# Performance work log

Hardware: AMD Instinct MI355X
Metric: run time of the kernel (lower is better)

The kernel has to match this reference:

```python
import jax, jax.numpy as jnp
import numpy as np

N_USER = 100000
N_ITEM = 100000
SUPP = 10000
B = 1024
L = 50
S = 256
H = 4
E = 64
HID = 64


def setup_inputs() -> dict:
    key = jax.random.key(0)
    ks = jax.random.split(key, 32)
    f32 = jnp.float32
    inp = {}
    # forward int args
    inp["x"] = jax.random.randint(ks[0], (B, 2), 0, N_USER)
    inp["src_his"] = jax.random.randint(ks[1], (B, L), 0, N_ITEM)
    inp["src_hl"] = jax.random.randint(ks[2], (B,), 0, L)
    inp["tgt_his"] = jax.random.randint(ks[3], (B, L), 0, N_ITEM)
    inp["tgt_hl"] = jax.random.randint(ks[4], (B,), 0, L)
    # precomputed neighbor sampling: [2 get_user_emb calls, H heads, B, S]
    inp["sample_idx"] = jax.random.randint(ks[5], (2, H, B, S), 0, SUPP)
    inp["supp_users"] = jax.random.randint(ks[6], (SUPP,), 0, N_USER)
    # embedding tables (xavier-ish small scale)
    inp["src_user_emb"] = jax.random.normal(ks[7], (N_USER, E), f32) * 0.1
    inp["src_item_emb"] = jax.random.normal(ks[8], (N_ITEM, E), f32) * 0.1
    inp["tgt_user_emb"] = jax.random.normal(ks[9], (N_USER, E), f32) * 0.1
    inp["tgt_item_emb"] = jax.random.normal(ks[10], (N_ITEM, E), f32) * 0.1
    # attention / aggregation weights, stored [in, out]
    s = 1.0 / np.sqrt(E)
    inp["W_att_w"] = jax.random.normal(ks[11], (E, E), f32) * s
    inp["W_att_b"] = jnp.full((E,), 0.1, f32)
    inp["W_agg_w"] = jax.random.normal(ks[12], (E, E), f32) * s
    # per-head GAT projections, batched over heads
    inp["Wq"] = jax.random.normal(ks[13], (H, E, E), f32) * s
    inp["Wk"] = jax.random.normal(ks[14], (H, E, E), f32) * s
    inp["Wv"] = jax.random.normal(ks[15], (H, E, E), f32) * s
    inp["W_out"] = jax.random.normal(ks[16], (H * E, E), f32) * (1.0 / np.sqrt(H * E))
    # scoring MLP
    inp["l1_w"] = jax.random.normal(ks[17], (2 * E, HID), f32) * (1.0 / np.sqrt(2 * E))
    inp["l1_b"] = jnp.full((HID,), 0.1, f32)
    inp["l2_w"] = jax.random.normal(ks[18], (HID, E), f32) * (1.0 / np.sqrt(HID))
    inp["l2_b"] = jnp.full((E,), 0.1, f32)
    inp["l3_w"] = jax.random.normal(ks[19], (E, 1), f32) * s
    inp["l3_b"] = jnp.full((1,), 0.1, f32)
    return inp


def reference(x, src_his, src_hl, tgt_his, tgt_hl, sample_idx, supp_users,
              src_user_emb, src_item_emb, tgt_user_emb, tgt_item_emb,
              W_att_w, W_att_b, W_agg_w, Wq, Wk, Wv, W_out,
              l1_w, l1_b, l2_w, l2_b, l3_w, l3_b):
    user_id = x[:, 0]
    item_id = x[:, 1]

    def user_fea_encode(his, hl, user_table):
        # NOTE: original always gathers from src_model.item_embedding (even for tgt)
        Lh = his.shape[1]
        valid = jnp.arange(Lh)[None, :] < hl[:, None]          # [B,L]
        hist = src_item_emb[his] * valid[..., None]             # [B,L,E], padded rows zeroed
        u = user_table[user_id]                                 # [B,E]
        keyt = jnp.tanh(hist @ W_att_w + W_att_b)               # [B,L,E]
        pad = hist.sum(-1) == 0                                 # [B,L]
        att = jnp.einsum('ble,be->bl', keyt, u)
        # faithful masked_softmax: masked scores set to 0 BEFORE exp (exp(0)=1 still contributes)
        att = jnp.where(pad, 0.0, att)
        e = jnp.exp(att)
        att = e / (jnp.sum(e, axis=1, keepdims=True) + 1e-12)
        out = jnp.einsum('bl,ble->be', att, hist)
        return out @ W_agg_w                                    # W_agg has no bias

    def get_user_emb(fea, idx):
        # idx: [H,B,S] indices into supp_users; all heads batched in one einsum chain
        neigh = tgt_user_emb[supp_users[idx]]                   # [H,B,S,E]
        q = jnp.einsum('be,heo->hbo', fea, Wq)                  # [H,B,O]
        k = jnp.einsum('hbse,heo->hbso', neigh, Wk)             # [H,B,S,O]
        attn = jax.nn.softmax(jnp.einsum('hbo,hbso->hbs', q, k), axis=-1)
        ctx = jnp.einsum('hbs,hbso->hbo', attn, k)              # weighted sum over neighbors
        g = jnp.einsum('hbo,hop->hbp', ctx, Wv)                 # [H,B,O]
        g = jnp.transpose(g, (1, 0, 2)).reshape(fea.shape[0], -1)  # concat heads -> [B,H*O]
        return g @ W_out

    user_src_fea = user_fea_encode(src_his, src_hl, src_user_emb)
    user_emb = get_user_emb(user_src_fea, sample_idx[0])
    item_emb = tgt_item_emb[item_id]
    user_tgt_fea = user_fea_encode(tgt_his, tgt_hl, tgt_user_emb)
    hybrid_tgt_emb = get_user_emb(user_tgt_fea, sample_idx[1])

    x_t = jnp.concatenate([hybrid_tgt_emb, item_emb], axis=1)
    x1_t = jnp.tanh(x_t @ l1_w + l1_b)
    x2_t = jnp.tanh(x1_t @ l2_w + l2_b)
    x3_t = (x2_t @ l3_w + l3_b).reshape(-1)

    output = jnp.sum(user_emb * item_emb, axis=1)
    out_emb_s = user_emb * item_emb
    # (output, output_t, out_emb_s, out_emb_t); train=False branch (sim/domain heads are None)
    return (output, x3_t, out_emb_s, x2_t)
```

## Files before the change

### kernel.cpp

```cpp
#include <hip/hip_runtime.h>

constexpr int B    = 1024;
constexpr int L    = 50;
constexpr int S    = 256;
constexpr int H    = 4;
constexpr int E    = 64;
constexpr int HID  = 64;
constexpr int SUPP = 10000;

__device__ __forceinline__ float tanh_fast(float x) {
    const float xc = fminf(fmaxf(x, -15.0f), 15.0f);
    const float e  = __expf(2.0f * xc);
    return (e - 1.0f) * __builtin_amdgcn_rcpf(e + 1.0f);
}

__device__ __forceinline__ float lanebc(float v, int l) {
    return __int_as_float(__builtin_amdgcn_readlane(__float_as_int(v), l));
}

__global__ __launch_bounds__(256) void pre_kernel(
    const int* __restrict__ x,
    const int* __restrict__ src_his,
    const int* __restrict__ src_hl,
    const int* __restrict__ tgt_his,
    const int* __restrict__ tgt_hl,
    const float* __restrict__ item_emb,
    const float* __restrict__ src_user_emb,
    const float* __restrict__ tgt_user_emb,
    const int* __restrict__ supp_users,
    const float* __restrict__ W_att_w,
    const float* __restrict__ W_att_b,
    const float* __restrict__ W_agg_w,
    const float* __restrict__ Wq,
    const float* __restrict__ Wk,
    float* __restrict__ qout,
    float* __restrict__ K_supp)
{
    const int tid  = threadIdx.x;
    const int lane = tid & 63;
    const int wave = tid >> 6;

    if (blockIdx.y == 2) {
        const int h = wave;
        float wcol[E];
#pragma unroll
        for (int i = 0; i < E; i++) wcol[i] = Wk[h * E * E + i * E + lane];

        int j = blockIdx.x;
        float ev = tgt_user_emb[(size_t)supp_users[j] * E + lane];
#pragma unroll 1
        while (j < SUPP) {
            const int jn = j + (int)gridDim.x;
            float evn = 0.0f;
            if (jn < SUPP)
                evn = tgt_user_emb[(size_t)supp_users[jn] * E + lane];
            float a0 = 0.f, a1 = 0.f, a2 = 0.f, a3 = 0.f;
#pragma unroll
            for (int i = 0; i < E; i += 4) {
                a0 = fmaf(lanebc(ev, i + 0), wcol[i + 0], a0);
                a1 = fmaf(lanebc(ev, i + 1), wcol[i + 1], a1);
                a2 = fmaf(lanebc(ev, i + 2), wcol[i + 2], a2);
                a3 = fmaf(lanebc(ev, i + 3), wcol[i + 3], a3);
            }
            K_supp[((size_t)h * SUPP + j) * E + lane] = (a0 + a1) + (a2 + a3);
            j = jn;
            ev = evn;
        }
        return;
    }

    __shared__ float sHist[L * E];
    __shared__ float sAtt[64];
    __shared__ float sPart[4][E];
    __shared__ float sOut[E];

    const int b    = blockIdx.x;
    const int call = blockIdx.y;

    const int* his = call ? tgt_his : src_his;
    const int* hl  = call ? tgt_hl  : src_hl;
    const float* user_table = call ? tgt_user_emb : src_user_emb;

    float wcol[E];
#pragma unroll
    for (int i = 0; i < E; i++) wcol[i] = W_att_w[i * E + lane];

    const int uid    = x[2 * b];
    const float uv   = user_table[(size_t)uid * E + lane];
    const float bias = W_att_b[lane];
    const int hlen   = hl[b];

#pragma unroll 1
    for (int l = wave; l < L; l += 4)
        if (l >= hlen && lane == 0) sAtt[l] = 0.0f;

    if (wave < hlen) {
        int l = wave;
        float hv = item_emb[(size_t)his[b * L + l] * E + lane];
#pragma unroll 1
        while (true) {
            const int ln = l + 4;
            float hvn = 0.0f;
            if (ln < hlen)
                hvn = item_emb[(size_t)his[b * L + ln] * E + lane];
            sHist[l * E + lane] = hv;
            float a0 = bias, a1 = 0.f, a2 = 0.f, a3 = 0.f;
#pragma unroll
            for (int i = 0; i < E; i += 4) {
                a0 = fmaf(lanebc(hv, i + 0), wcol[i + 0], a0);
                a1 = fmaf(lanebc(hv, i + 1), wcol[i + 1], a1);
                a2 = fmaf(lanebc(hv, i + 2), wcol[i + 2], a2);
                a3 = fmaf(lanebc(hv, i + 3), wcol[i + 3], a3);
            }
            float part = tanh_fast((a0 + a1) + (a2 + a3)) * uv;
#pragma unroll
            for (int off = 32; off; off >>= 1) part += __shfl_xor(part, off);
            if (lane == 0) sAtt[l] = part;
            l = ln;
            if (l >= hlen) break;
            hv = hvn;
        }
    }
    __syncthreads();

    const float vex = (lane < L) ? __expf(sAtt[lane]) : 0.0f;
    float sden = vex;
#pragma unroll
    for (int off = 32; off; off >>= 1) sden += __shfl_xor(sden, off);
    const float rden = __builtin_amdgcn_rcpf(sden + 1e-12f);

    float c = 0.0f;
#pragma unroll 1
    for (int l = wave; l < hlen; l += 4)
        c = fmaf(lanebc(vex, l) * rden, sHist[l * E + lane], c);
    sPart[wave][lane] = c;
    __syncthreads();
    if (tid < E) sOut[tid] = sPart[0][tid] + sPart[1][tid] + sPart[2][tid] + sPart[3][tid];
    __syncthreads();

    float g = 0.0f;
#pragma unroll
    for (int k = 0; k < 16; k++) {
        const int i = wave * 16 + k;
        g += sOut[i] * W_agg_w[i * E + lane];
    }
    sPart[wave][lane] = g;
    __syncthreads();

    const float fval = sPart[0][lane] + sPart[1][lane] + sPart[2][lane] + sPart[3][lane];
    const float* Wqh = Wq + wave * E * E;
    float q0 = 0.f, q1 = 0.f, q2 = 0.f, q3 = 0.f;
#pragma unroll
    for (int i = 0; i < E; i += 4) {
        q0 = fmaf(lanebc(fval, i + 0), Wqh[(i + 0) * E + lane], q0);
        q1 = fmaf(lanebc(fval, i + 1), Wqh[(i + 1) * E + lane], q1);
        q2 = fmaf(lanebc(fval, i + 2), Wqh[(i + 2) * E + lane], q2);
        q3 = fmaf(lanebc(fval, i + 3), Wqh[(i + 3) * E + lane], q3);
    }
    qout[(((call * H) + wave) * B + b) * E + lane] = (q0 + q1) + (q2 + q3);
}

__global__ __launch_bounds__(256) void attn_kernel(
    const int* __restrict__ sample_idx,
    const float* __restrict__ K_supp,
    const float* __restrict__ qarr,
    const float* __restrict__ Wv,
    float* __restrict__ gout)
{
    __shared__ float sRed[8];
    __shared__ float sCtx[4][E];
    __shared__ float sC[E];
    __shared__ float sG[4][E];

    const int n    = blockIdx.x;
    const int xcd  = n & 7;
    const int h    = xcd >> 1;
    const int call = xcd & 1;
    const int b    = n >> 3;
    const int tid  = threadIdx.x;
    const int lane = tid & 63;
    const int wave = tid >> 6;
    const int u    = lane & 15;
    const int rsub = lane >> 4;
    const int s0   = wave * 64;

    const int* idx = sample_idx + (((call * H) + h) * B + b) * S;
    const float* Kh = K_supp + (size_t)h * SUPP * E;
    const float4 qu = *(const float4*)(qarr + ((size_t)(((call * H) + h) * B + b)) * E + 4 * u);

    int jr[16];
#pragma unroll
    for (int i = 0; i < 16; i++) jr[i] = idx[s0 + 4 * i + rsub];
    float4 kreg[16];
#pragma unroll
    for (int i = 0; i < 16; i++)
        kreg[i] = *(const float4*)(Kh + (size_t)jr[i] * E + 4 * u);

    float mylogit = 0.0f;
#pragma unroll
    for (int i = 0; i < 16; i++) {
        float part = kreg[i].x * qu.x + kreg[i].y * qu.y
                   + kreg[i].z * qu.z + kreg[i].w * qu.w;
#pragma unroll
        for (int off = 1; off < 16; off <<= 1) part += __shfl_xor(part, off);
        mylogit = (u == i) ? part : mylogit;
    }

    float m = mylogit;
#pragma unroll
    for (int off = 32; off; off >>= 1) m = fmaxf(m, __shfl_xor(m, off));
    if (lane == 0) sRed[wave] = m;
    __syncthreads();
    const float mx = fmaxf(fmaxf(sRed[0], sRed[1]), fmaxf(sRed[2], sRed[3]));
    const float ex = __expf(mylogit - mx);
    float sm = ex;
#pragma unroll
    for (int off = 32; off; off >>= 1) sm += __shfl_xor(sm, off);
    if (lane == 0) sRed[4 + wave] = sm;
    __syncthreads();
    const float denom = sRed[4] + sRed[5] + sRed[6] + sRed[7];
    const float pval = ex / denom;

    float4 cacc = make_float4(0.0f, 0.0f, 0.0f, 0.0f);
#pragma unroll
    for (int i = 0; i < 16; i++) {
        const float p = __shfl(pval, (lane & 48) + i);
        cacc.x += p * kreg[i].x;
        cacc.y += p * kreg[i].y;
        cacc.z += p * kreg[i].z;
        cacc.w += p * kreg[i].w;
    }
#pragma unroll
    for (int off = 16; off <= 32; off <<= 1) {
        cacc.x += __shfl_xor(cacc.x, off);
        cacc.y += __shfl_xor(cacc.y, off);
        cacc.z += __shfl_xor(cacc.z, off);
        cacc.w += __shfl_xor(cacc.w, off);
    }
    if (lane < 16) *(float4*)(&sCtx[wave][u * 4]) = cacc;
    __syncthreads();
    if (wave == 0) {
        sC[lane] = sCtx[0][lane] + sCtx[1][lane] + sCtx[2][lane] + sCtx[3][lane];
    }
    __syncthreads();

    const float* Wvh = Wv + h * E * E;
    float g = 0.0f;
#pragma unroll
    for (int k = 0; k < 16; k++) {
        const int c = wave * 16 + k;
        g += sC[c] * Wvh[c * E + lane];
    }
    sG[wave][lane] = g;
    __syncthreads();
    if (wave == 0) {
        gout[((size_t)(call * B) + b) * (H * E) + h * E + lane] =
            sG[0][lane] + sG[1][lane] + sG[2][lane] + sG[3][lane];
    }
}

__global__ __launch_bounds__(256) void final_kernel(
    const int* __restrict__ x,
    const float* __restrict__ tgt_item_emb,
    const float* __restrict__ gsrc,
    const float* __restrict__ gtgt,
    const float* __restrict__ W_out,
    const float* __restrict__ l1_w,
    const float* __restrict__ l1_b,
    const float* __restrict__ l2_w,
    const float* __restrict__ l2_b,
    const float* __restrict__ l3_w,
    const float* __restrict__ l3_b,
    float* __restrict__ out)
{
    __shared__ float sPart[4][E];
    __shared__ float sHyb[E];
    __shared__ float sItem[E];
    __shared__ float sX1[HID];

    const int b    = blockIdx.x;
    const int tid  = threadIdx.x;
    const int lane = tid & 63;
    const int wave = tid >> 6;

    if (tid < E) {
        const int item = x[2 * b + 1];
        sItem[tid] = tgt_item_emb[(size_t)item * E + tid];
    }

    const float* grow = (wave < 2) ? (gsrc + (size_t)b * (H * E))
                                   : (gtgt + (size_t)b * (H * E));
    const int i0 = (wave & 1) * 128;
    {
        const float4* g4 = (const float4*)(grow + i0);
        float a0 = 0.0f, a1 = 0.0f, a2 = 0.0f, a3 = 0.0f;
#pragma unroll
        for (int k = 0; k < 32; k++) {
            const float4 v = g4[k];
            const float* wr = W_out + (i0 + 4 * k) * E + lane;
            a0 += v.x * wr[0];
            a1 += v.y * wr[E];
            a2 += v.z * wr[2 * E];
            a3 += v.w * wr[3 * E];
        }
        sPart[wave][lane] = (a0 + a1) + (a2 + a3);
    }
    __syncthreads();

    if (wave == 0) {
        const float ue = sPart[0][lane] + sPart[1][lane];
        const float prod = ue * sItem[lane];
        out[2 * B + b * E + lane] = prod;
        float s = prod;
#pragma unroll
        for (int off = 32; off; off >>= 1) s += __shfl_xor(s, off);
        if (lane == 0) out[b] = s;
    }
    if (wave == 1) {
        sHyb[lane] = sPart[2][lane] + sPart[3][lane];
    }
    __syncthreads();

    float a1 = 0.0f;
#pragma unroll
    for (int k = 0; k < 32; k++) {
        const int i = wave * 32 + k;
        const float v = (i < 64) ? sHyb[i] : sItem[i - 64];
        a1 += v * l1_w[i * HID + lane];
    }
    sPart[wave][lane] = a1;
    __syncthreads();

    if (wave == 0) {
        const float a = l1_b[lane] + sPart[0][lane] + sPart[1][lane]
                      + sPart[2][lane] + sPart[3][lane];
        sX1[lane] = tanh_fast(a);
    }
    __syncthreads();

    if (wave == 0) {
        float a = l2_b[lane];
#pragma unroll
        for (int i = 0; i < HID; i++) a += sX1[i] * l2_w[i * E + lane];
        const float x2 = tanh_fast(a);
        out[2 * B + B * E + b * E + lane] = x2;
        float p = x2 * l3_w[lane];
#pragma unroll
        for (int off = 32; off; off >>= 1) p += __shfl_xor(p, off);
        if (lane == 0) out[B + b] = p + l3_b[0];
    }
}

extern "C" void kernel_launch(void* const* d_in, const int* in_sizes, int n_in,
                              void* d_out, int out_size, void* d_ws, size_t ws_size,
                              hipStream_t stream) {
    const int*   x            = (const int*)d_in[0];
    const int*   src_his      = (const int*)d_in[1];
    const int*   src_hl       = (const int*)d_in[2];
    const int*   tgt_his      = (const int*)d_in[3];
    const int*   tgt_hl       = (const int*)d_in[4];
    const int*   sample_idx   = (const int*)d_in[5];
    const int*   supp_users   = (const int*)d_in[6];
    const float* src_user_emb = (const float*)d_in[7];
    const float* src_item_emb = (const float*)d_in[8];
    const float* tgt_user_emb = (const float*)d_in[9];
    const float* tgt_item_emb = (const float*)d_in[10];
    const float* W_att_w      = (const float*)d_in[11];
    const float* W_att_b      = (const float*)d_in[12];
    const float* W_agg_w      = (const float*)d_in[13];
    const float* Wq           = (const float*)d_in[14];
    const float* Wk           = (const float*)d_in[15];
    const float* Wv           = (const float*)d_in[16];
    const float* W_out        = (const float*)d_in[17];
    const float* l1_w         = (const float*)d_in[18];
    const float* l1_b         = (const float*)d_in[19];
    const float* l2_w         = (const float*)d_in[20];
    const float* l2_b         = (const float*)d_in[21];
    const float* l3_w         = (const float*)d_in[22];
    const float* l3_b         = (const float*)d_in[23];

    float* ws      = (float*)d_ws;
    float* qarr    = ws;
    float* K_supp  = qarr + 2 * H * B * E;
    float* garr    = K_supp + H * SUPP * E;
    float* out     = (float*)d_out;

    pre_kernel<<<dim3(B, 3), 256, 0, stream>>>(
        x, src_his, src_hl, tgt_his, tgt_hl, src_item_emb,
        src_user_emb, tgt_user_emb, supp_users,
        W_att_w, W_att_b, W_agg_w, Wq, Wk, qarr, K_supp);
    attn_kernel<<<dim3(B * H * 2), 256, 0, stream>>>(
        sample_idx, K_supp, qarr, Wv, garr);
    final_kernel<<<dim3(B), 256, 0, stream>>>(
        x, tgt_item_emb, garr, garr + B * H * E, W_out,
        l1_w, l1_b, l2_w, l2_b, l3_w, l3_b, out);
}
```

Baseline: 261.9 us.

## Stage weight matrices in shared memory instead of per-lane register columns

Both the K_supp projection branch and the history-attention branch now load the 64x64 weight matrix into shared memory with float4 copies, rather than keeping a 64-float column per lane in registers. The input row is written to LDS and read back as broadcast float4s, replacing readlane broadcasts. The K_supp branch also changes its work split: each block now handles one head and a strided chunk of support users, so its stride is fixed at 1024, which assumes a 1024-block grid in that branch. The aim is to cut VGPR pressure to raise occupancy and to replace scalar readlanes with LDS loads, at the cost of extra LDS traffic, a 16KB shared buffer and added barriers.

```diff
diff --git a/kernel.cpp b/kernel.cpp
--- a/kernel.cpp
+++ b/kernel.cpp
@@ -36,31 +36,67 @@
     float* __restrict__ qout,
     float* __restrict__ K_supp)
 {
+    __shared__ __align__(16) float sW[E * E];
+    __shared__ __align__(16) float sHist[L * E];
+    __shared__ float sAtt[64];
+    __shared__ float sPart[4][E];
+    __shared__ float sOut[E];
+
     const int tid  = threadIdx.x;
     const int lane = tid & 63;
     const int wave = tid >> 6;
 
     if (blockIdx.y == 2) {
-        const int h = wave;
-        float wcol[E];
-#pragma unroll
-        for (int i = 0; i < E; i++) wcol[i] = Wk[h * E * E + i * E + lane];
-
-        int j = blockIdx.x;
+        const int h     = blockIdx.x & 3;
+        const int chunk = blockIdx.x >> 2;
+        {
+            const float4* wsrc = (const float4*)(Wk + h * E * E);
+            float4* wdst = (float4*)sW;
+#pragma unroll
+            for (int k = 0; k < 4; k++) wdst[tid + 256 * k] = wsrc[tid + 256 * k];
+        }
+        float* sEv = sHist;
+
+        int j = chunk + 256 * wave;
         float ev = tgt_user_emb[(size_t)supp_users[j] * E + lane];
+        __syncthreads();
+
 #pragma unroll 1
         while (j < SUPP) {
-            const int jn = j + (int)gridDim.x;
+            const int jn = j + 1024;
             float evn = 0.0f;
             if (jn < SUPP)
                 evn = tgt_user_emb[(size_t)supp_users[jn] * E + lane];
+            sEv[wave * E + lane] = ev;
+            const float4* e4 = (const float4*)&sEv[wave * E];
+
+            int lidx = lane;
+            asm volatile("" : "+v"(lidx));
+            const float* wl = sW + lidx;
+
             float a0 = 0.f, a1 = 0.f, a2 = 0.f, a3 = 0.f;
 #pragma unroll
-            for (int i = 0; i < E; i += 4) {
-                a0 = fmaf(lanebc(ev, i + 0), wcol[i + 0], a0);
-                a1 = fmaf(lanebc(ev, i + 1), wcol[i + 1], a1);
-                a2 = fmaf(lanebc(ev, i + 2), wcol[i + 2], a2);
-                a3 = fmaf(lanebc(ev, i + 3), wcol[i + 3], a3);
+            for (int k = 0; k < 4; k++) {
+                const float4 v0 = e4[k];
+                const float4 v1 = e4[k + 4];
+                const float4 v2 = e4[k + 8];
+                const float4 v3 = e4[k + 12];
+                a0 = fmaf(v0.x, wl[(4 * k + 0) * E], a0);
+                a0 = fmaf(v0.y, wl[(4 * k + 1) * E], a0);
+                a0 = fmaf(v0.z, wl[(4 * k + 2) * E], a0);
+                a0 = fmaf(v0.w, wl[(4 * k + 3) * E], a0);
+                a1 = fmaf(v1.x, wl[(16 + 4 * k + 0) * E], a1);
+                a1 = fmaf(v1.y, wl[(16 + 4 * k + 1) * E], a1);
+                a1 = fmaf(v1.z, wl[(16 + 4 * k + 2) * E], a1);
+                a1 = fmaf(v1.w, wl[(16 + 4 * k + 3) * E], a1);
+                a2 = fmaf(v2.x, wl[(32 + 4 * k + 0) * E], a2);
+                a2 = fmaf(v2.y, wl[(32 + 4 * k + 1) * E], a2);
+                a2 = fmaf(v2.z, wl[(32 + 4 * k + 2) * E], a2);
+                a2 = fmaf(v2.w, wl[(32 + 4 * k + 3) * E], a2);
+                a3 = fmaf(v3.x, wl[(48 + 4 * k + 0) * E], a3);
+                a3 = fmaf(v3.y, wl[(48 + 4 * k + 1) * E], a3);
+                a3 = fmaf(v3.z, wl[(48 + 4 * k + 2) * E], a3);
+                a3 = fmaf(v3.w, wl[(48 + 4 * k + 3) * E], a3);
             }
             K_supp[((size_t)h * SUPP + j) * E + lane] = (a0 + a1) + (a2 + a3);
             j = jn;
@@ -69,11 +105,6 @@
         return;
     }
 
-    __shared__ float sHist[L * E];
-    __shared__ float sAtt[64];
-    __shared__ float sPart[4][E];
-    __shared__ float sOut[E];
-
     const int b    = blockIdx.x;
     const int call = blockIdx.y;
 
@@ -81,9 +112,12 @@
     const int* hl  = call ? tgt_hl  : src_hl;
     const float* user_table = call ? tgt_user_emb : src_user_emb;
 
-    float wcol[E];
-#pragma unroll
-    for (int i = 0; i < E; i++) wcol[i] = W_att_w[i * E + lane];
+    {
+        const float4* wsrc = (const float4*)W_att_w;
+        float4* wdst = (float4*)sW;
+#pragma unroll
+        for (int k = 0; k < 4; k++) wdst[tid + 256 * k] = wsrc[tid + 256 * k];
+    }
 
     const int uid    = x[2 * b];
     const float uv   = user_table[(size_t)uid * E + lane];
@@ -93,6 +127,8 @@
 #pragma unroll 1
     for (int l = wave; l < L; l += 4)
         if (l >= hlen && lane == 0) sAtt[l] = 0.0f;
+
+    __syncthreads();
 
     if (wave < hlen) {
         int l = wave;
@@ -104,13 +140,35 @@
             if (ln < hlen)
                 hvn = item_emb[(size_t)his[b * L + ln] * E + lane];
             sHist[l * E + lane] = hv;
+            const float4* hrow = (const float4*)&sHist[l * E];
+
+            int lidx = lane;
+            asm volatile("" : "+v"(lidx));
+            const float* wl = sW + lidx;
+
             float a0 = bias, a1 = 0.f, a2 = 0.f, a3 = 0.f;
 #pragma unroll
-            for (int i = 0; i < E; i += 4) {
-                a0 = fmaf(lanebc(hv, i + 0), wcol[i + 0], a0);
-                a1 = fmaf(lanebc(hv, i + 1), wcol[i + 1], a1);
-                a2 = fmaf(lanebc(hv, i + 2), wcol[i + 2], a2);
-                a3 = fmaf(lanebc(hv, i + 3), wcol[i + 3], a3);
+            for (int k = 0; k < 4; k++) {
+                const float4 h0 = hrow[k];
+                const float4 h1 = hrow[k + 4];
+                const float4 h2 = hrow[k + 8];
+                const float4 h3 = hrow[k + 12];
+                a0 = fmaf(h0.x, wl[(4 * k + 0) * E], a0);
+                a0 = fmaf(h0.y, wl[(4 * k + 1) * E], a0);
+                a0 = fmaf(h0.z, wl[(4 * k + 2) * E], a0);
+                a0 = fmaf(h0.w, wl[(4 * k + 3) * E], a0);
+                a1 = fmaf(h1.x, wl[(16 + 4 * k + 0) * E], a1);
+                a1 = fmaf(h1.y, wl[(16 + 4 * k + 1) * E], a1);
+                a1 = fmaf(h1.z, wl[(16 + 4 * k + 2) * E], a1);
+                a1 = fmaf(h1.w, wl[(16 + 4 * k + 3) * E], a1);
+                a2 = fmaf(h2.x, wl[(32 + 4 * k + 0) * E], a2);
+                a2 = fmaf(h2.y, wl[(32 + 4 * k + 1) * E], a2);
+                a2 = fmaf(h2.z, wl[(32 + 4 * k + 2) * E], a2);
+                a2 = fmaf(h2.w, wl[(32 + 4 * k + 3) * E], a2);
+                a3 = fmaf(h3.x, wl[(48 + 4 * k + 0) * E], a3);
+                a3 = fmaf(h3.y, wl[(48 + 4 * k + 1) * E], a3);
+                a3 = fmaf(h3.z, wl[(48 + 4 * k + 2) * E], a3);
+                a3 = fmaf(h3.w, wl[(48 + 4 * k + 3) * E], a3);
             }
             float part = tanh_fast((a0 + a1) + (a2 + a3)) * uv;
 #pragma unroll
```

Result: no change. 259.8 us (-0.8%).
